# Kernel tuning notes

Hardware: AMD Instinct MI355X
Metric: run time of the kernel (lower is better)

## Reference

```python
import jax, jax.numpy as jnp
import numpy as np

N, E, B, H, L = 100000, 200000, 2048, 256, 4
EPS_MSG = 1e-7   # GENConv message eps
LN_EPS = 1e-5    # torch LayerNorm default eps
SM_EPS = 1e-16   # PyG softmax denominator eps


def layer_norm(x, g, b):
    mu = x.mean(-1, keepdims=True)
    var = ((x - mu) ** 2).mean(-1, keepdims=True)
    return (x - mu) * jax.lax.rsqrt(var + LN_EPS) * g + b


def gen_conv(x, src, dst, eattr, t, W1, b1, lg, lb, W2, b2):
    # GENConv(aggr='softmax', learn_t, num_layers=2, norm='layer')
    msg = jax.nn.relu(x[src] + eattr) + EPS_MSG                      # [E,H]
    scaled = msg * t
    seg_max = jax.ops.segment_max(scaled, dst, num_segments=N)       # [N,H]
    seg_max = jnp.where(jnp.isfinite(seg_max), seg_max, 0.0)
    ex = jnp.exp(scaled - seg_max[dst])                              # [E,H]
    denom = jax.ops.segment_sum(ex, dst, num_segments=N)             # [N,H]
    alpha = ex / (denom[dst] + SM_EPS)
    out = jax.ops.segment_sum(msg * alpha, dst, num_segments=N)      # [N,H]
    out = out + x                                                    # root residual inside GENConv
    h = jax.nn.relu(layer_norm(out @ W1 + b1, lg, lb))               # MLP: Lin -> LN -> ReLU -> Lin
    return h @ W2 + b2


def setup_inputs() -> dict:
    key = jax.random.key(0)
    ks = iter(jax.random.split(key, 16))
    s = lambda *sh: jax.random.normal(next(ks), sh, jnp.float32) * 0.05
    return dict(
        x=jax.random.normal(next(ks), (N, 9), jnp.float32),
        edge_index=jax.random.randint(next(ks), (2, E), 0, N),
        edge_attr=jax.random.normal(next(ks), (E, 3), jnp.float32),
        batch=jnp.sort(jax.random.randint(next(ks), (N,), 0, B)),
        node_W=s(9, H), node_b=jnp.zeros((H,), jnp.float32),
        edge_W=s(3, H), edge_b=jnp.zeros((H,), jnp.float32),
        vn_emb=jnp.zeros((1, H), jnp.float32),
        ln_g=jnp.ones((L, H), jnp.float32), ln_b=jnp.zeros((L, H), jnp.float32),
        t=jnp.ones((L - 1,), jnp.float32),
        mlp_W1=s(L - 1, H, 2 * H), mlp_b1=jnp.zeros((L - 1, 2 * H), jnp.float32),
        mlp_ln_g=jnp.ones((L - 1, 2 * H), jnp.float32), mlp_ln_b=jnp.zeros((L - 1, 2 * H), jnp.float32),
        mlp_W2=s(L - 1, 2 * H, H), mlp_b2=jnp.zeros((L - 1, H), jnp.float32),
    )


def reference(x, edge_index, edge_attr, batch, node_W, node_b, edge_W, edge_b,
              vn_emb, ln_g, ln_b, t, mlp_W1, mlp_b1, mlp_ln_g, mlp_ln_b, mlp_W2, mlp_b2):
    src, dst = edge_index[0], edge_index[1]
    h = x @ node_W + node_b                                          # node encoder
    ea = edge_attr @ edge_W + edge_b                                 # edge encoder
    vn = jnp.broadcast_to(vn_emb, (B, H))
    counts = jax.ops.segment_sum(jnp.ones((N,), h.dtype), batch, num_segments=B)
    inv_counts = (1.0 / jnp.maximum(counts, 1.0))[:, None]           # [B,1]
    # layers[1:] run conv (block='res+'); layers[0] supplies only the final norm+act
    for l in range(1, L):
        hn = jax.nn.relu(layer_norm(h, ln_g[l], ln_b[l]))            # dropout=0.1 is a no-op in eval
        h = h + gen_conv(hn, src, dst, ea, t[l - 1],
                         mlp_W1[l - 1], mlp_b1[l - 1], mlp_ln_g[l - 1], mlp_ln_b[l - 1],
                         mlp_W2[l - 1], mlp_b2[l - 1])
        vn = vn + jax.ops.segment_sum(h, batch, num_segments=B) * inv_counts  # scatter_mean
        h = h + vn[batch]                                            # broadcast virtual node
    h = jax.nn.relu(layer_norm(h, ln_g[0], ln_b[0]))
    return jax.ops.segment_sum(h, batch, num_segments=B) * inv_counts  # global_mean_pool [B,H]
```

## Files before the change

kernel.cpp:

```cpp
#include <hip/hip_runtime.h>
#include <cstdint>
#include <cstddef>


typedef _Float16 half8_t __attribute__((ext_vector_type(8)));
typedef _Float16 half4_t __attribute__((ext_vector_type(4)));
typedef float    floatx4 __attribute__((ext_vector_type(4)));

#define DEVINL __device__ __forceinline__

DEVINL float wave_sum(float v) {
#pragma unroll
  for (int m = 32; m; m >>= 1) v += __shfl_xor(v, m, 64);
  return v;
}

__global__ __launch_bounds__(256) void k_node_enc(
    const float* __restrict__ x, const float* __restrict__ W,
    const float* __restrict__ bias, _Float16* __restrict__ h, int Nr) {
  __shared__ float sW[9 * 256];
  __shared__ float sb[256];
  __shared__ float sx[72];
  const int j = threadIdx.x;
#pragma unroll
  for (int k = 0; k < 9; ++k) sW[k * 256 + j] = W[k * 256 + j];
  sb[j] = bias[j];
  const int row0 = blockIdx.x * 8;
  if (j < 72) {
    int p = row0 * 9 + j;
    sx[j] = (p < Nr * 9) ? x[p] : 0.f;
  }
  __syncthreads();
  for (int r = 0; r < 8; ++r) {
    int row = row0 + r;
    if (row >= Nr) break;
    float acc = sb[j];
#pragma unroll
    for (int k = 0; k < 9; ++k) acc = fmaf(sx[r * 9 + k], sW[k * 256 + j], acc);
    h[(size_t)row * 256 + j] = (_Float16)acc;
  }
}

__global__ void k_bptr(const int* __restrict__ batch, int* __restrict__ bptr,
                       int N_, int B_) {
  int b = blockIdx.x * 256 + threadIdx.x;
  if (b > B_) return;
  int lo = 0, hi = N_;
  while (lo < hi) {
    int mid = (lo + hi) >> 1;
    if (batch[mid] < b) lo = mid + 1; else hi = mid;
  }
  bptr[b] = lo;
}

__global__ void k_deg(const int* __restrict__ ei, int* __restrict__ deg, int E_) {
  int e = blockIdx.x * 256 + threadIdx.x;
  if (e < E_) atomicAdd(&deg[ei[E_ + e]], 1);
}

__global__ __launch_bounds__(256) void k_scan1(
    const int* __restrict__ in, int* __restrict__ out1, int* __restrict__ bsum, int n) {
  __shared__ int tmp[256];
  const int t = threadIdx.x;
  const int base = blockIdx.x * 1024;
  int v[4];
  int run = 0;
#pragma unroll
  for (int i = 0; i < 4; ++i) {
    int p = base + t * 4 + i;
    int xv = (p < n) ? in[p] : 0;
    run += xv;
    v[i] = run;
  }
  tmp[t] = run;
  __syncthreads();
  for (int off = 1; off < 256; off <<= 1) {
    int u = (t >= off) ? tmp[t - off] : 0;
    __syncthreads();
    tmp[t] += u;
    __syncthreads();
  }
  int excl = tmp[t] - run;
#pragma unroll
  for (int i = 0; i < 4; ++i) {
    int p = base + t * 4 + i;
    if (p < n) out1[p] = v[i] + excl;
  }
  if (t == 255) bsum[blockIdx.x] = tmp[255];
}

__global__ void k_scan2(int* bsum, int nb, int* ptr0) {
  if (threadIdx.x == 0 && blockIdx.x == 0) {
    int run = 0;
    for (int i = 0; i < nb; ++i) { int xv = bsum[i]; bsum[i] = run; run += xv; }
    ptr0[0] = 0;
  }
}

__global__ __launch_bounds__(256) void k_scan3(int* out1, const int* __restrict__ bsum, int n) {
  int add = bsum[blockIdx.x];
  int p0 = blockIdx.x * 1024 + threadIdx.x * 4;
#pragma unroll
  for (int i = 0; i < 4; ++i) {
    int p = p0 + i;
    if (p < n) out1[p] += add;
  }
}

__global__ void k_copy(const int* __restrict__ a, int* __restrict__ b, int n) {
  int i = blockIdx.x * 256 + threadIdx.x;
  if (i < n) b[i] = a[i];
}

__global__ void k_csrfill(const int* __restrict__ ei, int* __restrict__ cursor,
                          int* __restrict__ csr_src, int* __restrict__ csr_eid, int E_) {
  int e = blockIdx.x * 256 + threadIdx.x;
  if (e < E_) {
    int d = ei[E_ + e];
    int pos = atomicAdd(&cursor[d], 1);
    csr_src[pos] = ei[e];
    csr_eid[pos] = e;
  }
}

__global__ void k_vninit(const float* __restrict__ emb, float* __restrict__ vn) {
  vn[(size_t)blockIdx.x * 256 + threadIdx.x] = emb[threadIdx.x];
}

__global__ __launch_bounds__(256) void k_wcvt_all(
    const float* __restrict__ W1, const float* __restrict__ W2,
    _Float16* __restrict__ W1T, _Float16* __restrict__ W2T) {
  int idx = blockIdx.x * 256 + threadIdx.x;
  int mat = idx >> 17;
  int rem = idx & 131071;
  if (mat < 3) {
    int k = rem >> 9, n = rem & 511;
    W1T[(size_t)mat * 131072 + (size_t)n * 256 + k] =
        (_Float16)W1[(size_t)mat * 131072 + rem];
  } else {
    int m = mat - 3;
    int k = rem >> 8, n = rem & 255;
    W2T[(size_t)m * 131072 + (size_t)n * 512 + k] =
        (_Float16)W2[(size_t)m * 131072 + rem];
  }
}

template <int VN>
__global__ __launch_bounds__(256) void k_ln256(
    const _Float16* __restrict__ h, const float* __restrict__ vn,
    const int* __restrict__ batch, const float* __restrict__ g,
    const float* __restrict__ b, _Float16* __restrict__ out, int Nr) {
  int row = blockIdx.x * 4 + (threadIdx.x >> 6);
  if (row >= Nr) return;
  int lane = threadIdx.x & 63;
  half4_t xh = *(const half4_t*)(h + (size_t)row * 256 + lane * 4);
  float4 xv = {(float)xh[0], (float)xh[1], (float)xh[2], (float)xh[3]};
  if constexpr (VN) {
    int bb = batch[row];
    float4 vv = *(const float4*)(vn + (size_t)bb * 256 + lane * 4);
    xv.x += vv.x; xv.y += vv.y; xv.z += vv.z; xv.w += vv.w;
  }
  float s = wave_sum(xv.x + xv.y + xv.z + xv.w);
  float mu = s * (1.f / 256.f);
  float d0 = xv.x - mu, d1 = xv.y - mu, d2 = xv.z - mu, d3 = xv.w - mu;
  float v = wave_sum(d0 * d0 + d1 * d1 + d2 * d2 + d3 * d3);
  float rstd = rsqrtf(v * (1.f / 256.f) + 1e-5f);
  float4 gv = *(const float4*)(g + lane * 4);
  float4 bv = *(const float4*)(b + lane * 4);
  half4_t o;
  o[0] = (_Float16)fmaxf(d0 * rstd * gv.x + bv.x, 0.f);
  o[1] = (_Float16)fmaxf(d1 * rstd * gv.y + bv.y, 0.f);
  o[2] = (_Float16)fmaxf(d2 * rstd * gv.z + bv.z, 0.f);
  o[3] = (_Float16)fmaxf(d3 * rstd * gv.w + bv.w, 0.f);
  *(half4_t*)(out + (size_t)row * 256 + lane * 4) = o;
}

__global__ __launch_bounds__(256) void k_aggregate(
    const _Float16* __restrict__ hn, const float* __restrict__ eattr,
    const float* __restrict__ edgeW, const float* __restrict__ edgeB,
    const int* __restrict__ indptr, const int* __restrict__ csr_src,
    const int* __restrict__ csr_eid, const float* __restrict__ tptr,
    _Float16* __restrict__ agg, int Nr) {
  __shared__ float sW[4 * 256];
  const int tj = threadIdx.x;
  sW[tj] = edgeW[tj];
  sW[256 + tj] = edgeW[256 + tj];
  sW[512 + tj] = edgeW[512 + tj];
  sW[768 + tj] = edgeB[tj];
  __syncthreads();

  int node = blockIdx.x * 4 + (threadIdx.x >> 6);
  if (node >= Nr) return;
  int lane = threadIdx.x & 63;
  float tval = tptr[0];
  int e0 = indptr[node], e1 = indptr[node + 1];
  float M[4], D[4], Nu[4];
#pragma unroll
  for (int i = 0; i < 4; ++i) { M[i] = -1e38f; D[i] = 0.f; Nu[i] = 0.f; }
  for (int s = e0; s < e1; ++s) {
    int srcn = csr_src[s];
    int eid = csr_eid[s];
    float ex0 = eattr[(size_t)eid * 3 + 0];
    float ex1 = eattr[(size_t)eid * 3 + 1];
    float ex2 = eattr[(size_t)eid * 3 + 2];
    half4_t hv = *(const half4_t*)(hn + (size_t)srcn * 256 + lane * 4);
#pragma unroll
    for (int i = 0; i < 4; ++i) {
      int j = lane * 4 + i;
      float eaj = fmaf(ex0, sW[j], fmaf(ex1, sW[256 + j], fmaf(ex2, sW[512 + j], sW[768 + j])));
      float msg = fmaxf((float)hv[i] + eaj, 0.f) + 1e-7f;
      float sc = msg * tval;
      float nM = fmaxf(M[i], sc);
      float sOld = __expf(M[i] - nM);
      float pr = __expf(sc - nM);
      D[i] = D[i] * sOld + pr;
      Nu[i] = Nu[i] * sOld + pr * msg;
      M[i] = nM;
    }
  }
  half4_t hs = *(const half4_t*)(hn + (size_t)node * 256 + lane * 4);
  half4_t res;
#pragma unroll
  for (int i = 0; i < 4; ++i)
    res[i] = (_Float16)(Nu[i] / (D[i] + 1e-16f) + (float)hs[i]);
  *(half4_t*)(agg + (size_t)node * 256 + lane * 4) = res;
}

__global__ __launch_bounds__(256, 2) void k_gemm1(
    const _Float16* __restrict__ A, const _Float16* __restrict__ BT,
    const float* __restrict__ bias, _Float16* __restrict__ outh,
    float2* __restrict__ rstat, int M) {
  constexpr int K = 256, NN = 512, NT = K / 64;
  __shared__ _Float16 ldsA[128 * 64];
  __shared__ _Float16 ldsB[128 * 64];
  const int lane = threadIdx.x & 63;
  const int wv = threadIdx.x >> 6;
  const int m0 = blockIdx.y * 128;
  const int n0 = blockIdx.x * 128;
  const int wm = (wv >> 1) * 64;
  const int wn = (wv & 1) * 64;
  const int q = lane >> 4;
  const int l16 = lane & 15;
  floatx4 acc[4][4] = {};

  size_t offA[4], offB[4];
  int ldsOff[4];
#pragma unroll
  for (int i = 0; i < 4; ++i) {
    int p = (i * 4 + wv) * 64 + lane;
    int r = p >> 3;
    int s = p & 7;
    int g = s ^ (r & 7);
    int rowA = m0 + r;
    rowA = rowA < M ? rowA : (M - 1);
    offA[i] = (size_t)rowA * K + g * 8;
    offB[i] = (size_t)(n0 + r) * K + g * 8;
    ldsOff[i] = p * 8;
  }
  half8_t ra[4], rb[4];
  auto loadtile = [&](int kt) {
#pragma unroll
    for (int i = 0; i < 4; ++i) {
      ra[i] = *(const half8_t*)(A + offA[i] + kt);
      rb[i] = *(const half8_t*)(BT + offB[i] + kt);
    }
  };
  auto writetile = [&]() {
#pragma unroll
    for (int i = 0; i < 4; ++i) {
      *(half8_t*)(ldsA + ldsOff[i]) = ra[i];
      *(half8_t*)(ldsB + ldsOff[i]) = rb[i];
    }
  };

  loadtile(0);
  writetile();
#pragma unroll
  for (int t = 0; t < NT; ++t) {
    __syncthreads();
    if (t + 1 < NT) loadtile((t + 1) * 64);
#pragma unroll
    for (int kk = 0; kk < 2; ++kk) {
      half8_t af[4], bf[4];
      const int c8 = kk * 4 + q;
#pragma unroll
      for (int rt = 0; rt < 4; ++rt) {
        int r = wm + rt * 16 + l16;
        af[rt] = *(const half8_t*)(ldsA + (size_t)(r * 8 + (c8 ^ (r & 7))) * 8);
      }
#pragma unroll
      for (int ct = 0; ct < 4; ++ct) {
        int n = wn + ct * 16 + l16;
        bf[ct] = *(const half8_t*)(ldsB + (size_t)(n * 8 + (c8 ^ (n & 7))) * 8);
      }
#pragma unroll
      for (int rt = 0; rt < 4; ++rt)
#pragma unroll
        for (int ct = 0; ct < 4; ++ct)
          acc[rt][ct] = __builtin_amdgcn_mfma_f32_16x16x32_f16(af[rt], bf[ct], acc[rt][ct], 0, 0, 0);
    }
    __syncthreads();
    if (t + 1 < NT) writetile();
  }

#pragma unroll
  for (int rt = 0; rt < 4; ++rt) {
#pragma unroll
    for (int rr = 0; rr < 4; ++rr) {
      int row = m0 + wm + rt * 16 + q * 4 + rr;
      float vv[4];
      float s = 0.f, s2 = 0.f;
#pragma unroll
      for (int ct = 0; ct < 4; ++ct) {
        int col = n0 + wn + ct * 16 + l16;
        float v = acc[rt][ct][rr] + bias[col];
        vv[ct] = v;
        s += v;
        s2 += v * v;
      }
#pragma unroll
      for (int m = 1; m < 16; m <<= 1) {
        s += __shfl_xor(s, m, 64);
        s2 += __shfl_xor(s2, m, 64);
      }
      if (row < M) {
#pragma unroll
        for (int ct = 0; ct < 4; ++ct) {
          int col = n0 + wn + ct * 16 + l16;
          outh[(size_t)row * NN + col] = (_Float16)vv[ct];
        }
        if (l16 == 0) {
          atomicAdd(&rstat[row].x, s);
          atomicAdd(&rstat[row].y, s2);
        }
      }
    }
  }
}

template <int VN>
__global__ __launch_bounds__(256, 2) void k_gemm2(
    const _Float16* __restrict__ A, const _Float16* __restrict__ BT,
    const float* __restrict__ bias, const float2* __restrict__ rstat,
    const float* __restrict__ lg, const float* __restrict__ lb,
    const float* __restrict__ vn, const int* __restrict__ batch,
    _Float16* __restrict__ outf, int M) {
  constexpr int K = 512, NN = 256, NT = K / 64;
  constexpr int EPS = 68;
  __shared__ _Float16 ldsbuf[4 * 64 * EPS];
  _Float16* ldsA = ldsbuf;
  _Float16* ldsB = ldsbuf + 128 * 64;
  __shared__ float sg[512];
  __shared__ float sbt[512];
  const int tid = threadIdx.x;
  sg[tid] = lg[tid];
  sg[tid + 256] = lg[tid + 256];
  sbt[tid] = lb[tid];
  sbt[tid + 256] = lb[tid + 256];
  __syncthreads();

  const int lane = tid & 63;
  const int wv = tid >> 6;
  const int m0 = blockIdx.y * 128;
  const int n0 = blockIdx.x * 128;
  const int wm = (wv >> 1) * 64;
  const int wn = (wv & 1) * 64;
  const int q = lane >> 4;
  const int l16 = lane & 15;
  floatx4 acc[4][4] = {};

  size_t offA[4], offB[4];
  int ldsOff[4], gcolA[4];
  float aco[4], cco[4];
#pragma unroll
  for (int i = 0; i < 4; ++i) {
    int p = (i * 4 + wv) * 64 + lane;
    int r = p >> 3;
    int s = p & 7;
    int g = s ^ (r & 7);
    int rowA = m0 + r;
    rowA = rowA < M ? rowA : (M - 1);
    offA[i] = (size_t)rowA * K + g * 8;
    offB[i] = (size_t)(n0 + r) * K + g * 8;
    ldsOff[i] = p * 8;
    gcolA[i] = g * 8;
    float2 st = rstat[rowA];
    float mu = st.x * (1.f / 512.f);
    float var = st.y * (1.f / 512.f) - mu * mu;
    float rs = rsqrtf(var + 1e-5f);
    aco[i] = rs;
    cco[i] = -mu * rs;
  }
  half8_t ra[4], rb[4];
  auto loadtile = [&](int kt) {
#pragma unroll
    for (int i = 0; i < 4; ++i) {
      ra[i] = *(const half8_t*)(A + offA[i] + kt);
      rb[i] = *(const half8_t*)(BT + offB[i] + kt);
    }
  };
  auto writetile = [&](int kt) {
#pragma unroll
    for (int i = 0; i < 4; ++i) {
      int c0 = kt + gcolA[i];
      half8_t ya;
#pragma unroll
      for (int j = 0; j < 8; ++j) {
        float e = fmaf((float)ra[i][j], aco[i], cco[i]);
        float y = fmaf(e, sg[c0 + j], sbt[c0 + j]);
        ya[j] = (_Float16)fmaxf(y, 0.f);
      }
      *(half8_t*)(ldsA + ldsOff[i]) = ya;
      *(half8_t*)(ldsB + ldsOff[i]) = rb[i];
    }
  };

  loadtile(0);
  writetile(0);
#pragma unroll
  for (int t = 0; t < NT; ++t) {
    __syncthreads();
    if (t + 1 < NT) loadtile((t + 1) * 64);
#pragma unroll
    for (int kk = 0; kk < 2; ++kk) {
      half8_t af[4], bf[4];
      const int c8 = kk * 4 + q;
#pragma unroll
      for (int rt = 0; rt < 4; ++rt) {
        int r = wm + rt * 16 + l16;
        af[rt] = *(const half8_t*)(ldsA + (size_t)(r * 8 + (c8 ^ (r & 7))) * 8);
      }
#pragma unroll
      for (int ct = 0; ct < 4; ++ct) {
        int n = wn + ct * 16 + l16;
        bf[ct] = *(const half8_t*)(ldsB + (size_t)(n * 8 + (c8 ^ (n & 7))) * 8);
      }
#pragma unroll
      for (int rt = 0; rt < 4; ++rt)
#pragma unroll
        for (int ct = 0; ct < 4; ++ct)
          acc[rt][ct] = __builtin_amdgcn_mfma_f32_16x16x32_f16(af[rt], bf[ct], acc[rt][ct], 0, 0, 0);
    }
    __syncthreads();
    if (t + 1 < NT) writetile((t + 1) * 64);
  }

  _Float16* epi = ldsbuf + wv * (64 * EPS);
#pragma unroll
  for (int rt = 0; rt < 4; ++rt) {
#pragma unroll
    for (int rr = 0; rr < 4; ++rr) {
      int rloc = rt * 16 + q * 4 + rr;
      int row = m0 + wm + rloc;
      int rowc = row < M ? row : (M - 1);
      int bb = 0;
      if constexpr (VN) bb = batch[rowc];
#pragma unroll
      for (int ct = 0; ct < 4; ++ct) {
        int cloc = ct * 16 + l16;
        int col = n0 + wn + cloc;
        float v = acc[rt][ct][rr] + bias[col];
        if constexpr (VN) v += vn[(size_t)bb * 256 + col];
        epi[rloc * EPS + cloc] = (_Float16)v;
      }
    }
  }
#pragma unroll
  for (int it = 0; it < 8; ++it) {
    int rloc = it * 8 + (lane >> 3);
    int row = m0 + wm + rloc;
    if (row < M) {
      int c0 = (lane & 7) * 8;
      size_t gidx = (size_t)row * NN + n0 + wn + c0;
      half8_t hv = *(const half8_t*)(outf + gidx);
      half8_t ev = *(const half8_t*)(epi + rloc * EPS + c0);
      half8_t o;
#pragma unroll
      for (int j = 0; j < 8; ++j) o[j] = (_Float16)((float)hv[j] + (float)ev[j]);
      *(half8_t*)(outf + gidx) = o;
    }
  }
}

__global__ __launch_bounds__(256) void k_vnsum(
    const _Float16* __restrict__ h, float* __restrict__ vn,
    const int* __restrict__ bptr) {
  int b = blockIdx.x, j = threadIdx.x;
  int n0 = bptr[b], n1 = bptr[b + 1];
  float acc = 0.f;
  for (int n = n0; n < n1; ++n) acc += (float)h[(size_t)n * 256 + j];
  int c = n1 - n0;
  vn[(size_t)b * 256 + j] += acc * (1.f / (float)(c > 1 ? c : 1));
}

__global__ __launch_bounds__(256) void k_lnpool(
    const _Float16* __restrict__ h, const float* __restrict__ vn,
    const int* __restrict__ bptr, const float* __restrict__ g,
    const float* __restrict__ b, float* __restrict__ out) {
  __shared__ float red[3][256];
  int bb = blockIdx.x;
  int w = threadIdx.x >> 6;
  int lane = threadIdx.x & 63;
  int n0 = bptr[bb], n1 = bptr[bb + 1];
  float4 vv = *(const float4*)(vn + (size_t)bb * 256 + lane * 4);
  float4 gv = *(const float4*)(g + lane * 4);
  float4 bv = *(const float4*)(b + lane * 4);
  float a0 = 0.f, a1 = 0.f, a2 = 0.f, a3 = 0.f;
  for (int row = n0 + w; row < n1; row += 4) {
    half4_t xh = *(const half4_t*)(h + (size_t)row * 256 + lane * 4);
    float x0 = (float)xh[0] + vv.x, x1 = (float)xh[1] + vv.y;
    float x2 = (float)xh[2] + vv.z, x3 = (float)xh[3] + vv.w;
    float s = wave_sum(x0 + x1 + x2 + x3);
    float mu = s * (1.f / 256.f);
    float d0 = x0 - mu, d1 = x1 - mu, d2 = x2 - mu, d3 = x3 - mu;
    float v = wave_sum(d0 * d0 + d1 * d1 + d2 * d2 + d3 * d3);
    float rstd = rsqrtf(v * (1.f / 256.f) + 1e-5f);
    a0 += fmaxf(d0 * rstd * gv.x + bv.x, 0.f);
    a1 += fmaxf(d1 * rstd * gv.y + bv.y, 0.f);
    a2 += fmaxf(d2 * rstd * gv.z + bv.z, 0.f);
    a3 += fmaxf(d3 * rstd * gv.w + bv.w, 0.f);
  }
  if (w > 0) {
    red[w - 1][lane * 4 + 0] = a0;
    red[w - 1][lane * 4 + 1] = a1;
    red[w - 1][lane * 4 + 2] = a2;
    red[w - 1][lane * 4 + 3] = a3;
  }
  __syncthreads();
  if (w == 0) {
    int c = n1 - n0;
    float ic = 1.f / (float)(c > 1 ? c : 1);
#pragma unroll
    for (int k = 0; k < 3; ++k) {
      a0 += red[k][lane * 4 + 0];
      a1 += red[k][lane * 4 + 1];
      a2 += red[k][lane * 4 + 2];
      a3 += red[k][lane * 4 + 3];
    }
    float4 o = {a0 * ic, a1 * ic, a2 * ic, a3 * ic};
    *(float4*)(out + (size_t)bb * 256 + lane * 4) = o;
  }
}

extern "C" void kernel_launch(void* const* d_in, const int* in_sizes, int n_in,
                              void* d_out, int out_size, void* d_ws, size_t ws_size,
                              hipStream_t stream) {
  const float* x      = (const float*)d_in[0];
  const int*   ei     = (const int*)d_in[1];
  const float* eattr  = (const float*)d_in[2];
  const int*   batch  = (const int*)d_in[3];
  const float* nodeW  = (const float*)d_in[4];
  const float* nodeB  = (const float*)d_in[5];
  const float* edgeW  = (const float*)d_in[6];
  const float* edgeB  = (const float*)d_in[7];
  const float* vnemb  = (const float*)d_in[8];
  const float* lng    = (const float*)d_in[9];
  const float* lnb    = (const float*)d_in[10];
  const float* tparam = (const float*)d_in[11];
  const float* W1     = (const float*)d_in[12];
  const float* b1     = (const float*)d_in[13];
  const float* mlng   = (const float*)d_in[14];
  const float* mlnb   = (const float*)d_in[15];
  const float* W2     = (const float*)d_in[16];
  const float* b2     = (const float*)d_in[17];
  float* out = (float*)d_out;

  const int N = in_sizes[3];
  const int E = in_sizes[1] / 2;
  const int B = out_size / 256;

  char* p = (char*)d_ws;
  auto take = [&](size_t bytes) -> char* {
    char* r = p;
    p += (bytes + 255) & ~(size_t)255;
    return r;
  };
  _Float16*  h   = (_Float16*)take((size_t)N * 256 * 2);
  _Float16*  t1  = (_Float16*)take((size_t)N * 512 * 2);
  _Float16*  hn  = t1;
  _Float16*  agg = (_Float16*)take((size_t)N * 256 * 2);
  _Float16*  W1T = (_Float16*)take((size_t)3 * 512 * 256 * 2);
  _Float16*  W2T = (_Float16*)take((size_t)3 * 256 * 512 * 2);
  float2*    rstat = (float2*)take((size_t)3 * N * 8);
  float*     vn  = (float*)take((size_t)B * 256 * 4);
  int*       bptr   = (int*)take((size_t)(B + 1) * 4);
  int*       deg    = (int*)take((size_t)N * 4);
  int*       indptr = (int*)take((size_t)(N + 1) * 4);
  int*       cursor = (int*)take((size_t)N * 4);
  int*       csr_src = (int*)take((size_t)E * 4);
  int*       csr_eid = (int*)take((size_t)E * 4);
  int*       bsum    = (int*)take(512 * 4);
  (void)ws_size; (void)n_in;

  hipMemsetAsync(deg, 0, (size_t)N * 4, stream);
  hipMemsetAsync(rstat, 0, (size_t)3 * N * 8, stream);

  k_node_enc<<<(N + 7) / 8, 256, 0, stream>>>(x, nodeW, nodeB, h, N);
  k_bptr<<<(B + 256) / 256, 256, 0, stream>>>(batch, bptr, N, B);

  const int nbN = (N + 1023) / 1024;
  k_deg<<<(E + 255) / 256, 256, 0, stream>>>(ei, deg, E);
  k_scan1<<<nbN, 256, 0, stream>>>(deg, indptr + 1, bsum, N);
  k_scan2<<<1, 64, 0, stream>>>(bsum, nbN, indptr);
  k_scan3<<<nbN, 256, 0, stream>>>(indptr + 1, bsum, N);
  k_copy<<<(N + 255) / 256, 256, 0, stream>>>(indptr, cursor, N);
  k_csrfill<<<(E + 255) / 256, 256, 0, stream>>>(ei, cursor, csr_src, csr_eid, E);

  k_wcvt_all<<<3072, 256, 0, stream>>>(W1, W2, W1T, W2T);
  k_vninit<<<B, 256, 0, stream>>>(vnemb, vn);

  const int lnGrid = (N + 3) / 4;
  const int mTiles = (N + 127) / 128;
  for (int l = 1; l <= 3; ++l) {
    if (l == 1)
      k_ln256<0><<<lnGrid, 256, 0, stream>>>(
          h, nullptr, nullptr, lng + (size_t)l * 256, lnb + (size_t)l * 256, hn, N);
    else
      k_ln256<1><<<lnGrid, 256, 0, stream>>>(
          h, vn, batch, lng + (size_t)l * 256, lnb + (size_t)l * 256, hn, N);
    k_aggregate<<<lnGrid, 256, 0, stream>>>(hn, eattr, edgeW, edgeB, indptr, csr_src, csr_eid,
                                            tparam + (l - 1), agg, N);
    float2* rs = rstat + (size_t)(l - 1) * N;
    k_gemm1<<<dim3(4, mTiles), 256, 0, stream>>>(
        agg, W1T + (size_t)(l - 1) * 512 * 256, b1 + (size_t)(l - 1) * 512, t1, rs, N);
    if (l == 1)
      k_gemm2<0><<<dim3(2, mTiles), 256, 0, stream>>>(
          t1, W2T + (size_t)(l - 1) * 256 * 512, b2 + (size_t)(l - 1) * 256, rs,
          mlng + (size_t)(l - 1) * 512, mlnb + (size_t)(l - 1) * 512, nullptr, nullptr, h, N);
    else
      k_gemm2<1><<<dim3(2, mTiles), 256, 0, stream>>>(
          t1, W2T + (size_t)(l - 1) * 256 * 512, b2 + (size_t)(l - 1) * 256, rs,
          mlng + (size_t)(l - 1) * 512, mlnb + (size_t)(l - 1) * 512, vn, batch, h, N);
    k_vnsum<<<B, 256, 0, stream>>>(h, vn, bptr);
  }

  k_lnpool<<<B, 256, 0, stream>>>(h, vn, bptr, lng, lnb, out);
}
```

Before: 884.7 us.

## Make gemm1 compute full rows per block and drop rstat atomics

gemm1 now has each block own 128 rows across all 512 output columns. The whole 128x256 A tile stays resident in LDS while B tiles stream through, so A is loaded once instead of four times. Row sum and sum-of-squares are kept in registers and written directly, which removes the atomics, the memset and the per-layer rstat buffers. gemm2 is relaunched with a grouped grid so blocks sharing an M tile run together for better cache locality. The cost is larger LDS use (64KB for A plus the B tile), which lowers occupancy, and the gemm1 grid is four times smaller.

```diff
diff --git a/kernel.cpp b/kernel.cpp
--- a/kernel.cpp
+++ b/kernel.cpp
@@ -230,110 +230,139 @@
     const _Float16* __restrict__ A, const _Float16* __restrict__ BT,
     const float* __restrict__ bias, _Float16* __restrict__ outh,
     float2* __restrict__ rstat, int M) {
-  constexpr int K = 256, NN = 512, NT = K / 64;
-  __shared__ _Float16 ldsA[128 * 64];
+  __shared__ _Float16 ldsA[128 * 256];
   __shared__ _Float16 ldsB[128 * 64];
-  const int lane = threadIdx.x & 63;
-  const int wv = threadIdx.x >> 6;
-  const int m0 = blockIdx.y * 128;
-  const int n0 = blockIdx.x * 128;
-  const int wm = (wv >> 1) * 64;
-  const int wn = (wv & 1) * 64;
+  const int tid = threadIdx.x;
+  const int lane = tid & 63;
+  const int wv = tid >> 6;
+  const int m0 = blockIdx.x * 128;
+  const int wm = wv * 32;
   const int q = lane >> 4;
   const int l16 = lane & 15;
-  floatx4 acc[4][4] = {};
-
-  size_t offA[4], offB[4];
-  int ldsOff[4];
+
+  for (int g = 0; g < 4; ++g) {
+    half8_t tmp[4];
+    int ss[4];
+#pragma unroll
+    for (int i = 0; i < 4; ++i) {
+      int s = (g * 4 + i) * 256 + tid;
+      int r = s >> 5;
+      int c = (s & 31) ^ (r & 7);
+      int rowA = m0 + r;
+      rowA = rowA < M ? rowA : (M - 1);
+      tmp[i] = *(const half8_t*)(A + (size_t)rowA * 256 + c * 8);
+      ss[i] = s;
+    }
+#pragma unroll
+    for (int i = 0; i < 4; ++i)
+      *(half8_t*)(ldsA + (size_t)ss[i] * 8) = tmp[i];
+  }
+
+  size_t offB[4];
+  int ldsOffB[4];
 #pragma unroll
   for (int i = 0; i < 4; ++i) {
     int p = (i * 4 + wv) * 64 + lane;
     int r = p >> 3;
     int s = p & 7;
-    int g = s ^ (r & 7);
-    int rowA = m0 + r;
-    rowA = rowA < M ? rowA : (M - 1);
-    offA[i] = (size_t)rowA * K + g * 8;
-    offB[i] = (size_t)(n0 + r) * K + g * 8;
-    ldsOff[i] = p * 8;
-  }
-  half8_t ra[4], rb[4];
-  auto loadtile = [&](int kt) {
-#pragma unroll
-    for (int i = 0; i < 4; ++i) {
-      ra[i] = *(const half8_t*)(A + offA[i] + kt);
-      rb[i] = *(const half8_t*)(BT + offB[i] + kt);
-    }
+    int gg = s ^ (r & 7);
+    offB[i] = (size_t)r * 256 + gg * 8;
+    ldsOffB[i] = p * 8;
+  }
+  half8_t rb[4];
+  auto loadB = [&](int j) {
+    int n = j >> 2, t = j & 3;
+    size_t base = (size_t)n * 128 * 256 + t * 64;
+#pragma unroll
+    for (int i = 0; i < 4; ++i)
+      rb[i] = *(const half8_t*)(BT + base + offB[i]);
   };
-  auto writetile = [&]() {
-#pragma unroll
-    for (int i = 0; i < 4; ++i) {
-      *(half8_t*)(ldsA + ldsOff[i]) = ra[i];
-      *(half8_t*)(ldsB + ldsOff[i]) = rb[i];
-    }
+  auto writeB = [&]() {
+#pragma unroll
+    for (int i = 0; i < 4; ++i)
+      *(half8_t*)(ldsB + ldsOffB[i]) = rb[i];
   };
 
-  loadtile(0);
-  writetile();
-#pragma unroll
-  for (int t = 0; t < NT; ++t) {
+  floatx4 acc[2][8] = {};
+  float sA[2][4] = {}, s2A[2][4] = {};
+
+  loadB(0);
+  writeB();
+  for (int j = 0; j < 16; ++j) {
     __syncthreads();
-    if (t + 1 < NT) loadtile((t + 1) * 64);
+    if (j + 1 < 16) loadB(j + 1);
+    const int t = j & 3;
 #pragma unroll
     for (int kk = 0; kk < 2; ++kk) {
-      half8_t af[4], bf[4];
       const int c8 = kk * 4 + q;
-#pragma unroll
-      for (int rt = 0; rt < 4; ++rt) {
+      const int cg = t * 8 + c8;
+      half8_t af[2], bf[8];
+#pragma unroll
+      for (int rt = 0; rt < 2; ++rt) {
         int r = wm + rt * 16 + l16;
-        af[rt] = *(const half8_t*)(ldsA + (size_t)(r * 8 + (c8 ^ (r & 7))) * 8);
-      }
-#pragma unroll
-      for (int ct = 0; ct < 4; ++ct) {
-        int n = wn + ct * 16 + l16;
+        af[rt] = *(const half8_t*)(ldsA + (size_t)(r * 32 + (cg ^ (r & 7))) * 8);
+      }
+#pragma unroll
+      for (int ct = 0; ct < 8; ++ct) {
+        int n = ct * 16 + l16;
         bf[ct] = *(const half8_t*)(ldsB + (size_t)(n * 8 + (c8 ^ (n & 7))) * 8);
       }
 #pragma unroll
-      for (int rt = 0; rt < 4; ++rt)
-#pragma unroll
-        for (int ct = 0; ct < 4; ++ct)
+      for (int rt = 0; rt < 2; ++rt)
+#pragma unroll
+        for (int ct = 0; ct < 8; ++ct)
           acc[rt][ct] = __builtin_amdgcn_mfma_f32_16x16x32_f16(af[rt], bf[ct], acc[rt][ct], 0, 0, 0);
     }
     __syncthreads();
-    if (t + 1 < NT) writetile();
-  }
-
-#pragma unroll
-  for (int rt = 0; rt < 4; ++rt) {
+    if (j + 1 < 16) writeB();
+    if ((j & 3) == 3) {
+      int n = j >> 2;
+#pragma unroll
+      for (int rt = 0; rt < 2; ++rt) {
+#pragma unroll
+        for (int rr = 0; rr < 4; ++rr) {
+          int row = m0 + wm + rt * 16 + q * 4 + rr;
+          float vv[8];
+          float s = 0.f, s2 = 0.f;
+#pragma unroll
+          for (int ct = 0; ct < 8; ++ct) {
+            int col = n * 128 + ct * 16 + l16;
+            float v = acc[rt][ct][rr] + bias[col];
+            vv[ct] = v;
+            s += v;
+            s2 += v * v;
+          }
+          if (row < M) {
+#pragma unroll
+            for (int ct = 0; ct < 8; ++ct) {
+              int col = n * 128 + ct * 16 + l16;
+              outh[(size_t)row * 512 + col] = (_Float16)vv[ct];
+            }
+          }
+          sA[rt][rr] += s;
+          s2A[rt][rr] += s2;
+        }
+      }
+#pragma unroll
+      for (int rt = 0; rt < 2; ++rt)
+#pragma unroll
+        for (int ct = 0; ct < 8; ++ct)
+          acc[rt][ct] = floatx4{0.f, 0.f, 0.f, 0.f};
+    }
+  }
+
+#pragma unroll
+  for (int rt = 0; rt < 2; ++rt) {
 #pragma unroll
     for (int rr = 0; rr < 4; ++rr) {
-      int row = m0 + wm + rt * 16 + q * 4 + rr;
-      float vv[4];
-      float s = 0.f, s2 = 0.f;
-#pragma unroll
-      for (int ct = 0; ct < 4; ++ct) {
-        int col = n0 + wn + ct * 16 + l16;
-        float v = acc[rt][ct][rr] + bias[col];
-        vv[ct] = v;
-        s += v;
-        s2 += v * v;
-      }
+      float s = sA[rt][rr], s2 = s2A[rt][rr];
 #pragma unroll
       for (int m = 1; m < 16; m <<= 1) {
         s += __shfl_xor(s, m, 64);
         s2 += __shfl_xor(s2, m, 64);
       }
-      if (row < M) {
-#pragma unroll
-        for (int ct = 0; ct < 4; ++ct) {
-          int col = n0 + wn + ct * 16 + l16;
-          outh[(size_t)row * NN + col] = (_Float16)vv[ct];
-        }
-        if (l16 == 0) {
-          atomicAdd(&rstat[row].x, s);
-          atomicAdd(&rstat[row].y, s2);
-        }
-      }
+      int row = m0 + wm + rt * 16 + q * 4 + rr;
+      if (l16 == 0 && row < M) rstat[row] = make_float2(s, s2);
     }
   }
 }
@@ -347,6 +376,12 @@
     _Float16* __restrict__ outf, int M) {
   constexpr int K = 512, NN = 256, NT = K / 64;
   constexpr int EPS = 68;
+  const int g = blockIdx.x;
+  const int mI = blockIdx.y * 8 + (g & 7);
+  const int nI = g >> 3;
+  const int mT = (M + 127) >> 7;
+  if (mI >= mT) return;
+
   __shared__ _Float16 ldsbuf[4 * 64 * EPS];
   _Float16* ldsA = ldsbuf;
   _Float16* ldsB = ldsbuf + 128 * 64;
@@ -361,8 +396,8 @@
 
   const int lane = tid & 63;
   const int wv = tid >> 6;
-  const int m0 = blockIdx.y * 128;
-  const int n0 = blockIdx.x * 128;
+  const int m0 = mI * 128;
+  const int n0 = nI * 128;
   const int wm = (wv >> 1) * 64;
   const int wn = (wv & 1) * 64;
   const int q = lane >> 4;
@@ -377,13 +412,13 @@
     int p = (i * 4 + wv) * 64 + lane;
     int r = p >> 3;
     int s = p & 7;
-    int g = s ^ (r & 7);
+    int gg = s ^ (r & 7);
     int rowA = m0 + r;
     rowA = rowA < M ? rowA : (M - 1);
-    offA[i] = (size_t)rowA * K + g * 8;
-    offB[i] = (size_t)(n0 + r) * K + g * 8;
+    offA[i] = (size_t)rowA * K + gg * 8;
+    offB[i] = (size_t)(n0 + r) * K + gg * 8;
     ldsOff[i] = p * 8;
-    gcolA[i] = g * 8;
+    gcolA[i] = gg * 8;
     float2 st = rstat[rowA];
     float mu = st.x * (1.f / 512.f);
     float var = st.y * (1.f / 512.f) - mu * mu;
@@ -405,10 +440,10 @@
       int c0 = kt + gcolA[i];
       half8_t ya;
 #pragma unroll
-      for (int j = 0; j < 8; ++j) {
-        float e = fmaf((float)ra[i][j], aco[i], cco[i]);
-        float y = fmaf(e, sg[c0 + j], sbt[c0 + j]);
-        ya[j] = (_Float16)fmaxf(y, 0.f);
+      for (int jj = 0; jj < 8; ++jj) {
+        float e = fmaf((float)ra[i][jj], aco[i], cco[i]);
+        float y = fmaf(e, sg[c0 + jj], sbt[c0 + jj]);
+        ya[jj] = (_Float16)fmaxf(y, 0.f);
       }
       *(half8_t*)(ldsA + ldsOff[i]) = ya;
       *(half8_t*)(ldsB + ldsOff[i]) = rb[i];
@@ -476,7 +511,7 @@
       half8_t ev = *(const half8_t*)(epi + rloc * EPS + c0);
       half8_t o;
 #pragma unroll
-      for (int j = 0; j < 8; ++j) o[j] = (_Float16)((float)hv[j] + (float)ev[j]);
+      for (int jj = 0; jj < 8; ++jj) o[jj] = (_Float16)((float)hv[jj] + (float)ev[jj]);
       *(half8_t*)(outf + gidx) = o;
     }
   }
@@ -581,7 +616,7 @@
   _Float16*  agg = (_Float16*)take((size_t)N * 256 * 2);
   _Float16*  W1T = (_Float16*)take((size_t)3 * 512 * 256 * 2);
   _Float16*  W2T = (_Float16*)take((size_t)3 * 256 * 512 * 2);
-  float2*    rstat = (float2*)take((size_t)3 * N * 8);
+  float2*    rstat = (float2*)take((size_t)N * 8);
   float*     vn  = (float*)take((size_t)B * 256 * 4);
   int*       bptr   = (int*)take((size_t)(B + 1) * 4);
   int*       deg    = (int*)take((size_t)N * 4);
@@ -593,7 +628,6 @@
   (void)ws_size; (void)n_in;
 
   hipMemsetAsync(deg, 0, (size_t)N * 4, stream);
-  hipMemsetAsync(rstat, 0, (size_t)3 * N * 8, stream);
 
   k_node_enc<<<(N + 7) / 8, 256, 0, stream>>>(x, nodeW, nodeB, h, N);
   k_bptr<<<(B + 256) / 256, 256, 0, stream>>>(batch, bptr, N, B);
@@ -611,6 +645,7 @@
 
   const int lnGrid = (N + 3) / 4;
   const int mTiles = (N + 127) / 128;
+  const dim3 g2grid(16, (mTiles + 7) / 8);
   for (int l = 1; l <= 3; ++l) {
     if (l == 1)
       k_ln256<0><<<lnGrid, 256, 0, stream>>>(
@@ -620,16 +655,15 @@
           h, vn, batch, lng + (size_t)l * 256, lnb + (size_t)l * 256, hn, N);
     k_aggregate<<<lnGrid, 256, 0, stream>>>(hn, eattr, edgeW, edgeB, indptr, csr_src, csr_eid,
                                             tparam + (l - 1), agg, N);
-    float2* rs = rstat + (size_t)(l - 1) * N;
-    k_gemm1<<<dim3(4, mTiles), 256, 0, stream>>>(
-        agg, W1T + (size_t)(l - 1) * 512 * 256, b1 + (size_t)(l - 1) * 512, t1, rs, N);
+    k_gemm1<<<mTiles, 256, 0, stream>>>(
+        agg, W1T + (size_t)(l - 1) * 512 * 256, b1 + (size_t)(l - 1) * 512, t1, rstat, N);
     if (l == 1)
-      k_gemm2<0><<<dim3(2, mTiles), 256, 0, stream>>>(
-          t1, W2T + (size_t)(l - 1) * 256 * 512, b2 + (size_t)(l - 1) * 256, rs,
+      k_gemm2<0><<<g2grid, 256, 0, stream>>>(
+          t1, W2T + (size_t)(l - 1) * 256 * 512, b2 + (size_t)(l - 1) * 256, rstat,
           mlng + (size_t)(l - 1) * 512, mlnb + (size_t)(l - 1) * 512, nullptr, nullptr, h, N);
     else
-      k_gemm2<1><<<dim3(2, mTiles), 256, 0, stream>>>(
-          t1, W2T + (size_t)(l - 1) * 256 * 512, b2 + (size_t)(l - 1) * 256, rs,
+      k_gemm2<1><<<g2grid, 256, 0, stream>>>(
+          t1, W2T + (size_t)(l - 1) * 256 * 512, b2 + (size_t)(l - 1) * 256, rstat,
           mlng + (size_t)(l - 1) * 512, mlnb + (size_t)(l - 1) * 512, vn, batch, h, N);
     k_vnsum<<<B, 256, 0, stream>>>(h, vn, bptr);
   }
```

After: 857.9 us. 3.0% less time.
